# Kernel tuning notes

Measured on AMD Instinct MI355X. Metric: run time of the kernel, lower is better.

The kernel has to match this reference:

```python
import jax, jax.numpy as jnp
import numpy as np

B, N, D = 4, 4096, 1024
LN_EPS = 1e-5

def setup_inputs() -> dict:
    key = jax.random.key(0)
    ks = jax.random.split(key, 12)
    s = 1.0 / np.sqrt(D)
    return {
        "embeddings": jax.random.normal(ks[0], (B, N, D), dtype=jnp.float32),
        "edge_indices": jax.random.randint(ks[1], (2, 8192), 0, N, dtype=jnp.int64),
        "edge_times": jax.random.uniform(ks[2], (8192,), dtype=jnp.float32),
        "timestamps": jax.random.uniform(ks[3], (N,), dtype=jnp.float32),
        "Wq": jax.random.uniform(ks[4], (D, D), jnp.float32, -s, s),
        "bq": jax.random.uniform(ks[5], (D,), jnp.float32, -s, s),
        "Wk": jax.random.uniform(ks[6], (D, D), jnp.float32, -s, s),
        "bk": jax.random.uniform(ks[7], (D,), jnp.float32, -s, s),
        "Wv": jax.random.uniform(ks[8], (D, D), jnp.float32, -s, s),
        "bv": jax.random.uniform(ks[9], (D,), jnp.float32, -s, s),
        "gamma": jnp.ones((D,), jnp.float32),
        "beta": jnp.zeros((D,), jnp.float32),
    }

def reference(embeddings, edge_indices, edge_times, timestamps,
              Wq, bq, Wk, bk, Wv, bv, gamma, beta):
    # edge_indices / edge_times / timestamps are unused by the original forward.
    d = embeddings.shape[-1]
    q = jnp.einsum("bnd,ed->bne", embeddings, Wq) + bq   # [B,N,D]
    k = jnp.einsum("bnd,ed->bne", embeddings, Wk) + bk
    v = jnp.einsum("bnd,ed->bne", embeddings, Wv) + bv
    scores = jnp.einsum("bnd,bmd->bnm", q, k) / jnp.sqrt(jnp.asarray(d, embeddings.dtype))
    attn = jax.nn.softmax(scores, axis=-1)                # [B,N,N]
    attended = jnp.einsum("bnm,bmd->bnd", attn, v)
    x = embeddings + attended
    mu = jnp.mean(x, axis=-1, keepdims=True)
    var = jnp.mean(jnp.square(x - mu), axis=-1, keepdims=True)
    return gamma * (x - mu) * jax.lax.rsqrt(var + LN_EPS) + beta
```

## Files before the change

kernel.cpp:

```cpp
#include <hip/hip_runtime.h>
#include <hip/hip_fp8.h>

typedef unsigned short u16;
typedef unsigned char  u8;
typedef long long      i64;
using bf16x8 = __attribute__((ext_vector_type(8))) __bf16;
using f32x4  = __attribute__((ext_vector_type(4))) float;

__device__ __forceinline__ u16 f2bf(float f) {
    unsigned u = __builtin_bit_cast(unsigned, f);
    u += 0x7fffu + ((u >> 16) & 1u);
    return (u16)(u >> 16);
}
__device__ __forceinline__ float bf2f(u16 h) {
    unsigned u = ((unsigned)h) << 16;
    return __builtin_bit_cast(float, u);
}
__device__ __forceinline__ u8 f2fp8(float f) {
    __hip_fp8_e4m3 t(f);
    return t.__x;
}
__device__ __forceinline__ float wred_sum(float v) {
    #pragma unroll
    for (int o = 32; o; o >>= 1) v += __shfl_xor(v, o, 64);
    return v;
}

__device__ __forceinline__ void gl2lds16(const void* g, void* l) {
    __builtin_amdgcn_global_load_lds(
        (__attribute__((address_space(1))) void*)(g),
        (__attribute__((address_space(3))) void*)(l), 16, 0, 0);
}

__global__ __launch_bounds__(256)
void cast_bf16(const float* __restrict__ src, u16* __restrict__ dst, int n4) {
    int i = blockIdx.x * 256 + threadIdx.x;
    if (i < n4) {
        float4 f = ((const float4*)src)[i];
        ushort4 u;
        u.x = f2bf(f.x); u.y = f2bf(f.y); u.z = f2bf(f.z); u.w = f2bf(f.w);
        ((ushort4*)dst)[i] = u;
    }
}

__global__ __launch_bounds__(256)
void cast_v_fp8(const u16* __restrict__ src, u8* __restrict__ dst, int n8) {
    int i = blockIdx.x * 256 + threadIdx.x;
    if (i < n8) {
        ushort4 a = ((const ushort4*)src)[2 * i];
        ushort4 b = ((const ushort4*)src)[2 * i + 1];
        union { u8 c[8]; unsigned long long q; } r;
        r.c[0] = f2fp8(bf2f(a.x)); r.c[1] = f2fp8(bf2f(a.y));
        r.c[2] = f2fp8(bf2f(a.z)); r.c[3] = f2fp8(bf2f(a.w));
        r.c[4] = f2fp8(bf2f(b.x)); r.c[5] = f2fp8(bf2f(b.y));
        r.c[6] = f2fp8(bf2f(b.z)); r.c[7] = f2fp8(bf2f(b.w));
        ((unsigned long long*)dst)[i] = r.q;
    }
}

template<int MODE>
__global__ __launch_bounds__(512, 2)
void gemm256(const u16* __restrict__ A, const u16* __restrict__ Bt,
             u16* __restrict__ oQ, u16* __restrict__ oK, u16* __restrict__ oVt,
             const float* __restrict__ bQ, const float* __restrict__ bK,
             const float* __restrict__ bV,
             u8* __restrict__ oP, float* __restrict__ sums, const float scale)
{
    __shared__ u16 smem[65536];
    const int tid = threadIdx.x;
    const int wv = tid >> 6, lane = tid & 63;
    const int wm = wv >> 2, wn = wv & 3;
    const int row0 = blockIdx.x << 8, col0 = blockIdx.y << 8;

    const int srow = tid >> 2;
    const int scol = ((tid & 3) ^ ((tid >> 3) & 3)) << 3;
    const u16* gA = A  + (size_t)(row0 + srow) * 1024 + scol;
    const u16* gB = Bt + (size_t)(col0 + srow) * 1024 + scol;
    char* lds = (char*)smem;
    const int wvo = wv << 10;

    const int fr = lane & 15, g = lane >> 4;
    const int kc = (g ^ ((fr >> 1) & 3)) << 4;

    f32x4 acc[8][4];
    #pragma unroll
    for (int i = 0; i < 8; i++)
        #pragma unroll
        for (int j = 0; j < 4; j++) acc[i][j] = (f32x4){0.f, 0.f, 0.f, 0.f};

    #define SG_A(ts, sl) { \
        gl2lds16(gA + (ts) * 32,          lds + (sl) * 32768 + wvo); \
        gl2lds16(gA + 131072 + (ts) * 32, lds + (sl) * 32768 + 8192 + wvo); }
    #define SG_B(ts, sl) { \
        gl2lds16(gB + (ts) * 32,          lds + (sl) * 32768 + 16384 + wvo); \
        gl2lds16(gB + 131072 + (ts) * 32, lds + (sl) * 32768 + 24576 + wvo); }

    SG_A(0, 0); SG_B(0, 0);
    SG_A(1, 1); SG_B(1, 1);
    SG_A(2, 2); SG_B(2, 2);
    asm volatile("s_waitcnt vmcnt(8)" ::: "memory");
    __builtin_amdgcn_s_barrier();

    for (int t = 0; t < 32; ++t) {
        const int slot = t & 3;
        const int ts = (t + 3) & 31;
        const int ns = (t + 3) & 3;
        const char* Ab = lds + slot * 32768;
        const char* Bb = Ab + 16384;

        SG_A(ts, ns);
        bf16x8 bf[4], af[4];
        #pragma unroll
        for (int j = 0; j < 4; ++j)
            bf[j] = *(const bf16x8*)(Bb + (wn * 64 + 16 * j + fr) * 64 + kc);
        #pragma unroll
        for (int i = 0; i < 4; ++i)
            af[i] = *(const bf16x8*)(Ab + (wm * 128 + 16 * i + fr) * 64 + kc);
        __builtin_amdgcn_sched_barrier(0);
        __builtin_amdgcn_s_barrier();
        asm volatile("s_waitcnt lgkmcnt(0)" ::: "memory");
        __builtin_amdgcn_sched_barrier(0);
        __builtin_amdgcn_s_setprio(1);
        #pragma unroll
        for (int i = 0; i < 4; ++i)
            #pragma unroll
            for (int j = 0; j < 4; ++j)
                acc[i][j] = __builtin_amdgcn_mfma_f32_16x16x32_bf16(af[i], bf[j], acc[i][j], 0, 0, 0);
        __builtin_amdgcn_s_setprio(0);

        SG_B(ts, ns);
        bf16x8 af2[4];
        #pragma unroll
        for (int i = 0; i < 4; ++i)
            af2[i] = *(const bf16x8*)(Ab + (wm * 128 + 64 + 16 * i + fr) * 64 + kc);
        asm volatile("s_waitcnt vmcnt(8)" ::: "memory");
        __builtin_amdgcn_sched_barrier(0);
        __builtin_amdgcn_s_barrier();
        asm volatile("s_waitcnt lgkmcnt(0)" ::: "memory");
        __builtin_amdgcn_sched_barrier(0);
        __builtin_amdgcn_s_setprio(1);
        #pragma unroll
        for (int i = 0; i < 4; ++i)
            #pragma unroll
            for (int j = 0; j < 4; ++j)
                acc[i + 4][j] = __builtin_amdgcn_mfma_f32_16x16x32_bf16(af2[i], bf[j], acc[i + 4][j], 0, 0, 0);
        __builtin_amdgcn_s_setprio(0);
    }
    #undef SG_A
    #undef SG_B

    asm volatile("s_waitcnt vmcnt(0)" ::: "memory");

    const int rB = (lane >> 4) << 2, cB = lane & 15;

    if (MODE == 0) {
        const int sel = col0 >> 10;
        if (sel < 2) {
            const float* bias = (sel == 0) ? bQ : bK;
            u16* dst = (sel == 0) ? oQ : oK;
            #pragma unroll
            for (int i = 0; i < 8; i++) {
                #pragma unroll
                for (int j = 0; j < 4; j++) {
                    const int m0 = row0 + wm * 128 + 16 * i + rB;
                    const int e  = (col0 & 1023) + wn * 64 + 16 * j + cB;
                    const float bb = bias[e];
                    #pragma unroll
                    for (int t = 0; t < 4; t++)
                        dst[(size_t)(m0 + t) * 1024 + e] = f2bf(acc[i][j][t] + bb);
                }
            }
        } else {
            const int b      = row0 >> 12;
            const int n_base = row0 & 4095;
            const int e0     = col0 & 1023;
            __syncthreads();
            #pragma unroll
            for (int i = 0; i < 8; i++) {
                const int n_l0 = wm * 128 + 16 * i + rB;
                const int hq   = n_l0 >> 3;
                const int off  = n_l0 & 7;
                #pragma unroll
                for (int j = 0; j < 4; j++) {
                    const int e_p = wn * 64 + 16 * j + cB;
                    const int hp  = hq ^ (e_p & 7);
                    const float bb = bV[e0 + e_p];
                    ushort4 pk;
                    pk.x = f2bf(acc[i][j][0] + bb);
                    pk.y = f2bf(acc[i][j][1] + bb);
                    pk.z = f2bf(acc[i][j][2] + bb);
                    pk.w = f2bf(acc[i][j][3] + bb);
                    *(ushort4*)&smem[e_p * 256 + hp * 8 + off] = pk;
                }
            }
            __syncthreads();
            #pragma unroll
            for (int it = 0; it < 16; ++it) {
                const int idx = it * 512 + tid;
                const int er  = idx >> 5;
                const int c   = idx & 31;
                const int cc  = c ^ (er & 7);
                int4 v = *(const int4*)&smem[er * 256 + cc * 8];
                *(int4*)&oVt[(size_t)b * 4194304 +
                             (size_t)(e0 + er) * 4096 + n_base + c * 8] = v;
            }
        }
    } else {
        float psum[8][4];
        #pragma unroll
        for (int i = 0; i < 8; i++)
            #pragma unroll
            for (int t = 0; t < 4; t++) psum[i][t] = 0.f;

        #pragma unroll
        for (int i = 0; i < 8; i++) {
            const int m0 = row0 + wm * 128 + 16 * i + rB;
            #pragma unroll
            for (int j = 0; j < 4; j++) {
                const int c = col0 + wn * 64 + 16 * j + cB;
                #pragma unroll
                for (int t = 0; t < 4; t++) {
                    const float e = __expf(acc[i][j][t] * scale);
                    psum[i][t] += e;
                    oP[(size_t)(m0 + t) * 4096 + c] = f2fp8(e);
                }
            }
        }
        #pragma unroll
        for (int i = 0; i < 8; i++) {
            #pragma unroll
            for (int t = 0; t < 4; t++) {
                float v = psum[i][t];
                v += __shfl_xor(v, 1, 64);
                v += __shfl_xor(v, 2, 64);
                v += __shfl_xor(v, 4, 64);
                v += __shfl_xor(v, 8, 64);
                if (cB == 0)
                    atomicAdd(&sums[row0 + wm * 128 + 16 * i + rB + t], v);
            }
        }
    }
}

__global__ __launch_bounds__(512, 2)
void pv256(const u8* __restrict__ p0, const u8* __restrict__ p1,
           const u8* __restrict__ p2, const u8* __restrict__ p3,
           const u8* __restrict__ vt8, const float* __restrict__ sums,
           float* __restrict__ out)
{
    __shared__ u8 smem[131072];
    const int b = blockIdx.z;
    const u8* Pb = (b == 0) ? p0 : (b == 1) ? p1 : (b == 2) ? p2 : p3;
    const u8* Vb = vt8 + (size_t)b * 4194304;
    const float* sm = sums + (b << 12);
    float* Ob = out + (size_t)b * 4194304;

    const int tid = threadIdx.x;
    const int wv = tid >> 6, lane = tid & 63;
    const int wm = wv >> 2, wn = wv & 3;
    const int row0 = blockIdx.x << 8, col0 = blockIdx.y << 8;

    const int srow = tid >> 2;
    const int sc16 = ((tid & 3) ^ ((tid >> 3) & 3)) << 4;
    const u8* gA = Pb + (size_t)(row0 + srow) * 4096 + sc16;
    const u8* gB = Vb + (size_t)(col0 + srow) * 4096 + sc16;
    char* lds = (char*)smem;
    const int wvo = wv << 10;

    const int fr = lane & 15, g = lane >> 4;
    const int sw = (fr >> 1) & 3;
    const int g2 = g >> 1, h8 = (g & 1) << 3;
    const int pc0 = ((g2 ^ sw) << 4) + h8;
    const int pc1 = (((2 + g2) ^ sw) << 4) + h8;

    f32x4 acc[8][4];
    #pragma unroll
    for (int i = 0; i < 8; i++)
        #pragma unroll
        for (int j = 0; j < 4; j++) acc[i][j] = (f32x4){0.f, 0.f, 0.f, 0.f};

    #define PG_A(ts, sl) { \
        gl2lds16(gA + (ts) * 64,          lds + (sl) * 32768 + wvo); \
        gl2lds16(gA + 524288 + (ts) * 64, lds + (sl) * 32768 + 8192 + wvo); }
    #define PG_B(ts, sl) { \
        gl2lds16(gB + (ts) * 64,          lds + (sl) * 32768 + 16384 + wvo); \
        gl2lds16(gB + 524288 + (ts) * 64, lds + (sl) * 32768 + 24576 + wvo); }

    PG_A(0, 0); PG_B(0, 0);
    PG_A(1, 1); PG_B(1, 1);
    PG_A(2, 2); PG_B(2, 2);
    asm volatile("s_waitcnt vmcnt(8)" ::: "memory");
    __builtin_amdgcn_s_barrier();

    for (int t = 0; t < 64; ++t) {
        const int slot = t & 3;
        const int ts = (t + 3) & 63;
        const int ns = (t + 3) & 3;
        const char* Ab = lds + slot * 32768;
        const char* Bb = Ab + 16384;

        PG_A(ts, ns);
        i64 af[8], bf[4];
        #pragma unroll
        for (int i = 0; i < 8; ++i) af[i] = *(const i64*)(Ab + (wm * 128 + 16 * i + fr) * 64 + pc0);
        #pragma unroll
        for (int j = 0; j < 4; ++j) bf[j] = *(const i64*)(Bb + (wn * 64 + 16 * j + fr) * 64 + pc0);
        __builtin_amdgcn_sched_barrier(0);
        __builtin_amdgcn_s_barrier();
        asm volatile("s_waitcnt lgkmcnt(0)" ::: "memory");
        __builtin_amdgcn_sched_barrier(0);
        __builtin_amdgcn_s_setprio(1);
        #pragma unroll
        for (int i = 0; i < 8; ++i)
            #pragma unroll
            for (int j = 0; j < 4; ++j)
                acc[i][j] = __builtin_amdgcn_mfma_f32_16x16x32_fp8_fp8(af[i], bf[j], acc[i][j], 0, 0, 0);
        __builtin_amdgcn_s_setprio(0);

        PG_B(ts, ns);
        #pragma unroll
        for (int i = 0; i < 8; ++i) af[i] = *(const i64*)(Ab + (wm * 128 + 16 * i + fr) * 64 + pc1);
        #pragma unroll
        for (int j = 0; j < 4; ++j) bf[j] = *(const i64*)(Bb + (wn * 64 + 16 * j + fr) * 64 + pc1);
        asm volatile("s_waitcnt vmcnt(8)" ::: "memory");
        __builtin_amdgcn_sched_barrier(0);
        __builtin_amdgcn_s_barrier();
        asm volatile("s_waitcnt lgkmcnt(0)" ::: "memory");
        __builtin_amdgcn_sched_barrier(0);
        __builtin_amdgcn_s_setprio(1);
        #pragma unroll
        for (int i = 0; i < 8; ++i)
            #pragma unroll
            for (int j = 0; j < 4; ++j)
                acc[i][j] = __builtin_amdgcn_mfma_f32_16x16x32_fp8_fp8(af[i], bf[j], acc[i][j], 0, 0, 0);
        __builtin_amdgcn_s_setprio(0);
    }
    #undef PG_A
    #undef PG_B

    asm volatile("s_waitcnt vmcnt(0)" ::: "memory");

    const int rB = (lane >> 4) << 2, cB = lane & 15;
    #pragma unroll
    for (int i = 0; i < 8; i++) {
        const int m0 = row0 + wm * 128 + 16 * i + rB;
        const float i0 = 1.0f / sm[m0];
        const float i1 = 1.0f / sm[m0 + 1];
        const float i2 = 1.0f / sm[m0 + 2];
        const float i3 = 1.0f / sm[m0 + 3];
        #pragma unroll
        for (int j = 0; j < 4; j++) {
            const int e = col0 + wn * 64 + 16 * j + cB;
            Ob[(size_t)(m0 + 0) * 1024 + e] = acc[i][j][0] * i0;
            Ob[(size_t)(m0 + 1) * 1024 + e] = acc[i][j][1] * i1;
            Ob[(size_t)(m0 + 2) * 1024 + e] = acc[i][j][2] * i2;
            Ob[(size_t)(m0 + 3) * 1024 + e] = acc[i][j][3] * i3;
        }
    }
}

__global__ __launch_bounds__(256)
void residual_ln(const float* __restrict__ emb, float* __restrict__ out,
                 const float* __restrict__ gamma, const float* __restrict__ beta) {
    const size_t row = blockIdx.x;
    const int t = threadIdx.x;
    const int wv = t >> 6, lane = t & 63;
    const size_t base = row * 1024 + t * 4;

    float4 ev = *(const float4*)(emb + base);
    float4 ov = *(const float4*)(out + base);
    float x0 = ev.x + ov.x, x1 = ev.y + ov.y, x2 = ev.z + ov.z, x3 = ev.w + ov.w;

    float s = x0 + x1 + x2 + x3;
    float q = x0 * x0 + x1 * x1 + x2 * x2 + x3 * x3;
    s = wred_sum(s);
    q = wred_sum(q);
    __shared__ float s1[4], s2[4];
    if (lane == 0) { s1[wv] = s; s2[wv] = q; }
    __syncthreads();
    s = s1[0] + s1[1] + s1[2] + s1[3];
    q = s2[0] + s2[1] + s2[2] + s2[3];

    const float mu  = s * (1.0f / 1024.0f);
    const float var = q * (1.0f / 1024.0f) - mu * mu;
    const float r   = rsqrtf(var + 1e-5f);

    float4 g  = *(const float4*)(gamma + t * 4);
    float4 be = *(const float4*)(beta + t * 4);
    float4 res;
    res.x = (x0 - mu) * r * g.x + be.x;
    res.y = (x1 - mu) * r * g.y + be.y;
    res.z = (x2 - mu) * r * g.z + be.z;
    res.w = (x3 - mu) * r * g.w + be.w;
    *(float4*)(out + base) = res;
}

extern "C" void kernel_launch(void* const* d_in, const int* in_sizes, int n_in,
                              void* d_out, int out_size, void* d_ws, size_t ws_size,
                              hipStream_t stream) {
    const float* emb   = (const float*)d_in[0];
    const float* Wq    = (const float*)d_in[4];
    const float* bq    = (const float*)d_in[5];
    const float* Wk    = (const float*)d_in[6];
    const float* bk    = (const float*)d_in[7];
    const float* Wv    = (const float*)d_in[8];
    const float* bv    = (const float*)d_in[9];
    const float* gamma = (const float*)d_in[10];
    const float* beta  = (const float*)d_in[11];
    float* out = (float*)d_out;

    char* ws = (char*)d_ws;
    if (ws_size < 140509184u) return;
    u16* Xbf = (u16*)(ws);
    u16* Wbf = (u16*)(ws + 33554432);
    u16* Qbf = (u16*)(ws + 39845888);
    u16* Kbf = (u16*)(ws + 73400320);
    u16* VTB = (u16*)(ws + 106954752);

    u8*    VT8  = (u8*)(ws);
    u8*    P0   = (u8*)(ws + 16777216);
    float* SUMS = (float*)(ws + 33554432);
    u8*    P1   = (u8*)(ws + 106954752);
    u8*    P2   = (u8*)(ws + 123731968);
    u8*    P3   = (u8*)(ws + 39845888);
    u8*    Pb[4] = {P0, P1, P2, P3};

    cast_bf16<<<16384, 256, 0, stream>>>(emb, Xbf, 4194304);
    cast_bf16<<<1024, 256, 0, stream>>>(Wq, Wbf,           262144);
    cast_bf16<<<1024, 256, 0, stream>>>(Wk, Wbf + 1048576, 262144);
    cast_bf16<<<1024, 256, 0, stream>>>(Wv, Wbf + 2097152, 262144);

    gemm256<0><<<dim3(64, 12), 512, 0, stream>>>(Xbf, Wbf,
        Qbf, Kbf, VTB, bq, bk, bv, nullptr, nullptr, 1.0f);

    cast_v_fp8<<<8192, 256, 0, stream>>>(VTB, VT8, 2097152);

    hipMemsetAsync(SUMS, 0, 65536, stream);

    for (int b = 0; b < 4; ++b) {
        const size_t o = (size_t)b * 4194304;
        gemm256<1><<<dim3(16, 16), 512, 0, stream>>>(Qbf + o, Kbf + o,
            nullptr, nullptr, nullptr, nullptr, nullptr, nullptr,
            Pb[b], SUMS + b * 4096, 0.03125f);
    }

    pv256<<<dim3(16, 4, 4), 512, 0, stream>>>(P0, P1, P2, P3, VT8, SUMS, out);

    residual_ln<<<16384, 256, 0, stream>>>(emb, out, gamma, beta);
}
```

Baseline: 589.5 us.

## Fuse V fp8 cast into QKV GEMM epilogue and batch score GEMMs

The QKV projection epilogue now quantizes V directly to fp8 and writes it transposed through a reswizzled LDS tile. This removes the intermediate bf16 V^T buffer and the separate cast kernel. The four per-batch score GEMM launches are merged into two launches using blockIdx.z over batch pairs, which cuts launch overhead and gives each launch a larger grid. The workspace layout is reshuffled so the P buffers do not overlap live data, and blockIdx.z is now also applied to the MODE 0 pointer offsets.

```diff
diff --git a/kernel.cpp b/kernel.cpp
--- a/kernel.cpp
+++ b/kernel.cpp
@@ -43,28 +43,14 @@
     }
 }
 
-__global__ __launch_bounds__(256)
-void cast_v_fp8(const u16* __restrict__ src, u8* __restrict__ dst, int n8) {
-    int i = blockIdx.x * 256 + threadIdx.x;
-    if (i < n8) {
-        ushort4 a = ((const ushort4*)src)[2 * i];
-        ushort4 b = ((const ushort4*)src)[2 * i + 1];
-        union { u8 c[8]; unsigned long long q; } r;
-        r.c[0] = f2fp8(bf2f(a.x)); r.c[1] = f2fp8(bf2f(a.y));
-        r.c[2] = f2fp8(bf2f(a.z)); r.c[3] = f2fp8(bf2f(a.w));
-        r.c[4] = f2fp8(bf2f(b.x)); r.c[5] = f2fp8(bf2f(b.y));
-        r.c[6] = f2fp8(bf2f(b.z)); r.c[7] = f2fp8(bf2f(b.w));
-        ((unsigned long long*)dst)[i] = r.q;
-    }
-}
-
 template<int MODE>
 __global__ __launch_bounds__(512, 2)
 void gemm256(const u16* __restrict__ A, const u16* __restrict__ Bt,
-             u16* __restrict__ oQ, u16* __restrict__ oK, u16* __restrict__ oVt,
+             u16* __restrict__ oQ, u16* __restrict__ oK,
              const float* __restrict__ bQ, const float* __restrict__ bK,
              const float* __restrict__ bV,
-             u8* __restrict__ oP, float* __restrict__ sums, const float scale)
+             u8* __restrict__ oP, u8* __restrict__ oP2,
+             float* __restrict__ sums, const float scale)
 {
     __shared__ u16 smem[65536];
     const int tid = threadIdx.x;
@@ -72,10 +58,11 @@
     const int wm = wv >> 2, wn = wv & 3;
     const int row0 = blockIdx.x << 8, col0 = blockIdx.y << 8;
 
+    const size_t boff = (size_t)blockIdx.z * 4194304;
     const int srow = tid >> 2;
     const int scol = ((tid & 3) ^ ((tid >> 3) & 3)) << 3;
-    const u16* gA = A  + (size_t)(row0 + srow) * 1024 + scol;
-    const u16* gB = Bt + (size_t)(col0 + srow) * 1024 + scol;
+    const u16* gA = A + boff + (size_t)(row0 + srow) * 1024 + scol;
+    const u16* gB = Bt + boff + (size_t)(col0 + srow) * 1024 + scol;
     char* lds = (char*)smem;
     const int wvo = wv << 10;
 
@@ -174,38 +161,39 @@
             const int b      = row0 >> 12;
             const int n_base = row0 & 4095;
             const int e0     = col0 & 1023;
+            unsigned* lds32 = (unsigned*)smem;
             __syncthreads();
             #pragma unroll
             for (int i = 0; i < 8; i++) {
                 const int n_l0 = wm * 128 + 16 * i + rB;
-                const int hq   = n_l0 >> 3;
-                const int off  = n_l0 & 7;
+                const int gq   = n_l0 >> 4;
+                const int kq   = (n_l0 >> 2) & 3;
                 #pragma unroll
                 for (int j = 0; j < 4; j++) {
                     const int e_p = wn * 64 + 16 * j + cB;
-                    const int hp  = hq ^ (e_p & 7);
                     const float bb = bV[e0 + e_p];
-                    ushort4 pk;
-                    pk.x = f2bf(acc[i][j][0] + bb);
-                    pk.y = f2bf(acc[i][j][1] + bb);
-                    pk.z = f2bf(acc[i][j][2] + bb);
-                    pk.w = f2bf(acc[i][j][3] + bb);
-                    *(ushort4*)&smem[e_p * 256 + hp * 8 + off] = pk;
+                    union { u8 c[4]; unsigned u; } pk;
+                    pk.c[0] = f2fp8(acc[i][j][0] + bb);
+                    pk.c[1] = f2fp8(acc[i][j][1] + bb);
+                    pk.c[2] = f2fp8(acc[i][j][2] + bb);
+                    pk.c[3] = f2fp8(acc[i][j][3] + bb);
+                    lds32[e_p * 64 + ((gq ^ (e_p & 15)) << 2) + kq] = pk.u;
                 }
             }
             __syncthreads();
             #pragma unroll
-            for (int it = 0; it < 16; ++it) {
+            for (int it = 0; it < 8; ++it) {
                 const int idx = it * 512 + tid;
-                const int er  = idx >> 5;
-                const int c   = idx & 31;
-                const int cc  = c ^ (er & 7);
-                int4 v = *(const int4*)&smem[er * 256 + cc * 8];
-                *(int4*)&oVt[(size_t)b * 4194304 +
-                             (size_t)(e0 + er) * 4096 + n_base + c * 8] = v;
+                const int er  = idx >> 4;
+                const int c16 = idx & 15;
+                int4 v = *(const int4*)&lds32[er * 64 + ((c16 ^ (er & 15)) << 2)];
+                *(int4*)&oP[(size_t)b * 4194304 +
+                            (size_t)(e0 + er) * 4096 + n_base + c16 * 16] = v;
             }
         }
     } else {
+        u8* Pz = blockIdx.z ? oP2 : oP;
+        float* smz = sums + (blockIdx.z << 12);
         float psum[8][4];
         #pragma unroll
         for (int i = 0; i < 8; i++)
@@ -222,7 +210,7 @@
                 for (int t = 0; t < 4; t++) {
                     const float e = __expf(acc[i][j][t] * scale);
                     psum[i][t] += e;
-                    oP[(size_t)(m0 + t) * 4096 + c] = f2fp8(e);
+                    Pz[(size_t)(m0 + t) * 4096 + c] = f2fp8(e);
                 }
             }
         }
@@ -236,7 +224,7 @@
                 v += __shfl_xor(v, 4, 64);
                 v += __shfl_xor(v, 8, 64);
                 if (cB == 0)
-                    atomicAdd(&sums[row0 + wm * 128 + 16 * i + rB + t], v);
+                    atomicAdd(&smz[row0 + wm * 128 + 16 * i + rB + t], v);
             }
         }
     }
@@ -415,15 +403,13 @@
     u16* Wbf = (u16*)(ws + 33554432);
     u16* Qbf = (u16*)(ws + 39845888);
     u16* Kbf = (u16*)(ws + 73400320);
-    u16* VTB = (u16*)(ws + 106954752);
-
-    u8*    VT8  = (u8*)(ws);
-    u8*    P0   = (u8*)(ws + 16777216);
+
+    u8*    P0   = (u8*)(ws);
+    u8*    P1   = (u8*)(ws + 16777216);
     float* SUMS = (float*)(ws + 33554432);
-    u8*    P1   = (u8*)(ws + 106954752);
+    u8*    P3   = (u8*)(ws + 39845888);
+    u8*    VT8  = (u8*)(ws + 106954752);
     u8*    P2   = (u8*)(ws + 123731968);
-    u8*    P3   = (u8*)(ws + 39845888);
-    u8*    Pb[4] = {P0, P1, P2, P3};
 
     cast_bf16<<<16384, 256, 0, stream>>>(emb, Xbf, 4194304);
     cast_bf16<<<1024, 256, 0, stream>>>(Wq, Wbf,           262144);
@@ -431,18 +417,16 @@
     cast_bf16<<<1024, 256, 0, stream>>>(Wv, Wbf + 2097152, 262144);
 
     gemm256<0><<<dim3(64, 12), 512, 0, stream>>>(Xbf, Wbf,
-        Qbf, Kbf, VTB, bq, bk, bv, nullptr, nullptr, 1.0f);
-
-    cast_v_fp8<<<8192, 256, 0, stream>>>(VTB, VT8, 2097152);
+        Qbf, Kbf, bq, bk, bv, VT8, nullptr, nullptr, 1.0f);
 
     hipMemsetAsync(SUMS, 0, 65536, stream);
 
-    for (int b = 0; b < 4; ++b) {
-        const size_t o = (size_t)b * 4194304;
-        gemm256<1><<<dim3(16, 16), 512, 0, stream>>>(Qbf + o, Kbf + o,
-            nullptr, nullptr, nullptr, nullptr, nullptr, nullptr,
-            Pb[b], SUMS + b * 4096, 0.03125f);
-    }
+    gemm256<1><<<dim3(16, 16, 2), 512, 0, stream>>>(Qbf, Kbf,
+        nullptr, nullptr, nullptr, nullptr, nullptr,
+        P0, P1, SUMS, 0.03125f);
+    gemm256<1><<<dim3(16, 16, 2), 512, 0, stream>>>(Qbf + 2 * 4194304, Kbf + 2 * 4194304,
+        nullptr, nullptr, nullptr, nullptr, nullptr,
+        P2, P3, SUMS + 8192, 0.03125f);
 
     pv256<<<dim3(16, 4, 4), 512, 0, stream>>>(P0, P1, P2, P3, VT8, SUMS, out);
 
```

Result: faster. 524.8 us (-11.0%).
